# Performance work log

Measured on AMD Instinct MI355X. Metric: run time of the kernel, lower is better.

Reference implementation:

```python
import jax, jax.numpy as jnp
import numpy as np

N_NODES = 50000
N_EDGES = 600000
DIM = 128
NUM_CLASSES = 10
EPS = 1e-15
MAX_NORM = 1.0 - 1e-5  # keep points strictly inside the unit ball for artanh


def _norm(x):
    return jnp.maximum(jnp.linalg.norm(x, axis=-1, keepdims=True), EPS)


def logmap0(x):
    # Poincare ball, c=1: artanh(||x||) * x / ||x||
    n = _norm(x)
    return jnp.arctanh(jnp.minimum(n, MAX_NORM)) * x / n


def expmap0(u):
    # Poincare ball, c=1: tanh(||u||) * u / ||u||
    n = _norm(u)
    return jnp.tanh(n) * u / n


def hyp_conv(x, W, b, src, dst):
    t = logmap0(x)                       # [N, D] manifold -> tangent at origin
    h = t @ W.T + b                      # [N, D] linear in tangent space
    y = expmap0(h)                       # [N, D] back to manifold
    # message passing: gather source features, scatter-add at destinations
    return jax.ops.segment_sum(y[src], dst, num_segments=N_NODES)


def setup_inputs() -> dict:
    key = jax.random.key(0)
    ks = jax.random.split(key, 8)
    edge_index = jax.random.randint(ks[0], (2, N_EDGES), 0, N_NODES, dtype=jnp.int64)
    # entity embeddings: small tangent vectors mapped onto the ball
    x = expmap0(0.01 * jax.random.normal(ks[1], (N_NODES, DIM), dtype=jnp.float32))
    s = 1.0 / np.sqrt(DIM)
    W1 = jax.random.normal(ks[2], (DIM, DIM), dtype=jnp.float32) * s
    b1 = jax.random.normal(ks[3], (DIM,), dtype=jnp.float32) * 0.01
    W2 = jax.random.normal(ks[4], (DIM, DIM), dtype=jnp.float32) * s
    b2 = jax.random.normal(ks[5], (DIM,), dtype=jnp.float32) * 0.01
    Wc = jax.random.normal(ks[6], (NUM_CLASSES, DIM), dtype=jnp.float32) * s
    bc = jax.random.normal(ks[7], (NUM_CLASSES,), dtype=jnp.float32) * 0.01
    return {"edge_index": edge_index, "x": x, "W1": W1, "b1": b1,
            "W2": W2, "b2": b2, "Wc": Wc, "bc": bc}


def reference(edge_index, x, W1, b1, W2, b2, Wc, bc):
    src, dst = edge_index[0], edge_index[1]
    h = hyp_conv(x, W1, b1, src, dst)
    h = jax.nn.relu(h)
    h = hyp_conv(h, W2, b2, src, dst)
    h = jax.nn.relu(h)
    t = logmap0(h)
    return t @ Wc.T + bc  # [N_NODES, NUM_CLASSES]
```

## Files before the change

kernel.cpp:

```cpp
#include <hip/hip_runtime.h>

#define N_NODES 50000
#define N_EDGES 600000
#define DIM 128
#define NCLS 10
#define ELLW 64
#define CURSTRIDE 16
#define EPSF 1e-15f
#define MAXNORM 0.99999f
#define NTILE ((N_NODES + 63) / 64)
#define FILL_BLOCKS 586
#define XFORM_BLOCKS 512

typedef __attribute__((ext_vector_type(8))) short bf16x8;
typedef __attribute__((ext_vector_type(4))) float f32x4;

__device__ inline float waveSum(float v) {
#pragma unroll
  for (int o = 1; o < 64; o <<= 1) v += __shfl_xor(v, o, 64);
  return v;
}

__device__ inline unsigned short f2bf(float f) {
  union { float f; unsigned u; } c; c.f = f;
  return (unsigned short)((c.u + 0x7FFFu + ((c.u >> 16) & 1u)) >> 16);
}
__device__ inline float bf_lo(unsigned u) {
  union { unsigned u; float f; } c; c.u = u << 16; return c.f;
}
__device__ inline float bf_hi(unsigned u) {
  union { unsigned u; float f; } c; c.u = u & 0xFFFF0000u; return c.f;
}

__global__ __launch_bounds__(256) void init_kernel(
    int* __restrict__ cursor, const float* __restrict__ W1, const float* __restrict__ W2,
    unsigned short* __restrict__ W1b, unsigned short* __restrict__ W2b)
{
  int i = blockIdx.x * 256 + threadIdx.x;
  if (i < N_NODES) cursor[i * CURSTRIDE] = 0;
  if (i < DIM * DIM) {
    W1b[i] = f2bf(W1[i]);
    W2b[i] = f2bf(W2[i]);
  }
}

__global__ __launch_bounds__(256, 2) void fill_transform(
    const int* __restrict__ src, const int* __restrict__ dst,
    int* __restrict__ cursor, int* __restrict__ ell,
    const float* __restrict__ x, const unsigned short* __restrict__ Wb,
    const float* __restrict__ b, unsigned short* __restrict__ y)
{
  __shared__ __align__(16) unsigned short At[64 * DIM];

  if (blockIdx.x < FILL_BLOCKS) {
    const int nthr = FILL_BLOCKS * 256;
    const int e = blockIdx.x * 256 + threadIdx.x;
    const int e0 = e, e1 = e + nthr, e2 = e + 2 * nthr, e3 = e + 3 * nthr;
    int d0, d1, d2, d3, s0, s1, s2, s3;
    if (e0 < N_EDGES) { d0 = dst[e0]; s0 = src[e0]; }
    if (e1 < N_EDGES) { d1 = dst[e1]; s1 = src[e1]; }
    if (e2 < N_EDGES) { d2 = dst[e2]; s2 = src[e2]; }
    if (e3 < N_EDGES) { d3 = dst[e3]; s3 = src[e3]; }
    int p0, p1, p2, p3;
    if (e0 < N_EDGES) p0 = atomicAdd(&cursor[d0 * CURSTRIDE], 1);
    if (e1 < N_EDGES) p1 = atomicAdd(&cursor[d1 * CURSTRIDE], 1);
    if (e2 < N_EDGES) p2 = atomicAdd(&cursor[d2 * CURSTRIDE], 1);
    if (e3 < N_EDGES) p3 = atomicAdd(&cursor[d3 * CURSTRIDE], 1);
    if (e0 < N_EDGES) ell[d0 * ELLW + p0] = s0;
    if (e1 < N_EDGES) ell[d1 * ELLW + p1] = s1;
    if (e2 < N_EDGES) ell[d2 * ELLW + p2] = s2;
    if (e3 < N_EDGES) ell[d3 * ELLW + p3] = s3;
    return;
  }

  const int tid = threadIdx.x;
  const int w = tid >> 6;
  const int l = tid & 63;
  const int lr = l & 15;
  const int lg = l >> 4;

  bf16x8 bf[8][4];
#pragma unroll
  for (int n = 0; n < 8; ++n)
#pragma unroll
    for (int kc = 0; kc < 4; ++kc)
      bf[n][kc] = *(const bf16x8*)(Wb + (n * 16 + lr) * DIM + kc * 32 + lg * 8);

  float bias[8];
#pragma unroll
  for (int n = 0; n < 8; ++n) bias[n] = b[n * 16 + lr];

  const int row = w * 16 + lr;

  for (int tile = blockIdx.x - FILL_BLOCKS; tile < NTILE; tile += XFORM_BLOCKS) {
    const int base = tile * 64;
    const int node = base + row;
    __syncthreads();

    float v[32];
    if (node < N_NODES) {
      const float4* xr = (const float4*)(x + (size_t)node * DIM + lg * 32);
#pragma unroll
      for (int q = 0; q < 8; ++q) {
        float4 f = xr[q];
        v[q * 4 + 0] = f.x; v[q * 4 + 1] = f.y; v[q * 4 + 2] = f.z; v[q * 4 + 3] = f.w;
      }
    } else {
#pragma unroll
      for (int q = 0; q < 32; ++q) v[q] = 0.f;
    }
    float sq = 0.f;
#pragma unroll
    for (int q = 0; q < 32; ++q) sq += v[q] * v[q];
    sq += __shfl_xor(sq, 16, 64);
    sq += __shfl_xor(sq, 32, 64);
    float n1 = sqrtf(sq);
    float nc = fmaxf(n1, EPSF);
    float nm = fminf(nc, MAXNORM);
    float scale = 0.5f * logf((1.f + nm) / (1.f - nm)) / nc;
#pragma unroll
    for (int s = 0; s < 4; ++s) {
      unsigned short tmp[8];
#pragma unroll
      for (int e = 0; e < 8; ++e) tmp[e] = f2bf(v[s * 8 + e] * scale);
      int byte = row * 256 + lg * 64 + s * 16;
      byte ^= (row & 7) << 4;
      *(bf16x8*)((char*)At + byte) = *(const bf16x8*)tmp;
    }
    __syncthreads();

    f32x4 acc[8];
#pragma unroll
    for (int n = 0; n < 8; ++n) {
      acc[n][0] = bias[n]; acc[n][1] = bias[n]; acc[n][2] = bias[n]; acc[n][3] = bias[n];
    }
#pragma unroll
    for (int kc = 0; kc < 4; ++kc) {
      int arow = w * 16 + lr;
      int byte = arow * 256 + kc * 64 + lg * 16;
      byte ^= (arow & 7) << 4;
      bf16x8 af = *(const bf16x8*)((const char*)At + byte);
#pragma unroll
      for (int n = 0; n < 8; ++n)
        acc[n] = __builtin_amdgcn_mfma_f32_16x16x32_bf16(af, bf[n][kc], acc[n], 0, 0, 0);
    }

    float rs[4];
#pragma unroll
    for (int j = 0; j < 4; ++j) {
      float s2 = 0.f;
#pragma unroll
      for (int n = 0; n < 8; ++n) s2 += acc[n][j] * acc[n][j];
      s2 += __shfl_xor(s2, 1, 64);
      s2 += __shfl_xor(s2, 2, 64);
      s2 += __shfl_xor(s2, 4, 64);
      s2 += __shfl_xor(s2, 8, 64);
      float n2 = sqrtf(s2);
      float n2c = fmaxf(n2, EPSF);
      rs[j] = tanhf(n2c) / n2c;
    }
#pragma unroll
    for (int j = 0; j < 4; ++j) {
      int nrow = base + w * 16 + lg * 4 + j;
      if (nrow < N_NODES) {
        unsigned short* yr = y + (size_t)nrow * DIM + lr;
#pragma unroll
        for (int n = 0; n < 8; ++n) yr[n * 16] = f2bf(acc[n][j] * rs[j]);
      }
    }
  }
}

__global__ __launch_bounds__(256) void gatherT_kernel(
    const unsigned short* __restrict__ y, const int* __restrict__ cursor,
    const int* __restrict__ ell, unsigned short* __restrict__ tout)
{
  const int node = blockIdx.x * 4 + (threadIdx.x >> 6);
  if (node >= N_NODES) return;
  const int lane = threadIdx.x & 63;
  const int* lst = ell + node * ELLW;
  const int cnt = cursor[node * CURSTRIDE];
  float2 a0 = {0.f, 0.f}, a1 = {0.f, 0.f}, a2 = {0.f, 0.f}, a3 = {0.f, 0.f};
  int j = 0;
  for (; j + 7 < cnt; j += 8) {
    unsigned u0 = ((const unsigned*)(y + (size_t)lst[j    ] * DIM))[lane];
    unsigned u1 = ((const unsigned*)(y + (size_t)lst[j + 1] * DIM))[lane];
    unsigned u2 = ((const unsigned*)(y + (size_t)lst[j + 2] * DIM))[lane];
    unsigned u3 = ((const unsigned*)(y + (size_t)lst[j + 3] * DIM))[lane];
    unsigned u4 = ((const unsigned*)(y + (size_t)lst[j + 4] * DIM))[lane];
    unsigned u5 = ((const unsigned*)(y + (size_t)lst[j + 5] * DIM))[lane];
    unsigned u6 = ((const unsigned*)(y + (size_t)lst[j + 6] * DIM))[lane];
    unsigned u7 = ((const unsigned*)(y + (size_t)lst[j + 7] * DIM))[lane];
    a0.x += bf_lo(u0); a0.y += bf_hi(u0);
    a1.x += bf_lo(u1); a1.y += bf_hi(u1);
    a2.x += bf_lo(u2); a2.y += bf_hi(u2);
    a3.x += bf_lo(u3); a3.y += bf_hi(u3);
    a0.x += bf_lo(u4); a0.y += bf_hi(u4);
    a1.x += bf_lo(u5); a1.y += bf_hi(u5);
    a2.x += bf_lo(u6); a2.y += bf_hi(u6);
    a3.x += bf_lo(u7); a3.y += bf_hi(u7);
  }
  for (; j + 3 < cnt; j += 4) {
    unsigned u0 = ((const unsigned*)(y + (size_t)lst[j    ] * DIM))[lane];
    unsigned u1 = ((const unsigned*)(y + (size_t)lst[j + 1] * DIM))[lane];
    unsigned u2 = ((const unsigned*)(y + (size_t)lst[j + 2] * DIM))[lane];
    unsigned u3 = ((const unsigned*)(y + (size_t)lst[j + 3] * DIM))[lane];
    a0.x += bf_lo(u0); a0.y += bf_hi(u0);
    a1.x += bf_lo(u1); a1.y += bf_hi(u1);
    a2.x += bf_lo(u2); a2.y += bf_hi(u2);
    a3.x += bf_lo(u3); a3.y += bf_hi(u3);
  }
  for (; j < cnt; ++j) {
    unsigned u0 = ((const unsigned*)(y + (size_t)lst[j] * DIM))[lane];
    a0.x += bf_lo(u0); a0.y += bf_hi(u0);
  }
  float2 r;
  r.x = fmaxf((a0.x + a1.x) + (a2.x + a3.x), 0.f);
  r.y = fmaxf((a0.y + a1.y) + (a2.y + a3.y), 0.f);

  float s = waveSum(r.x * r.x + r.y * r.y);
  float n = sqrtf(s);
  float nc = fmaxf(n, EPSF);
  float nm = fminf(nc, MAXNORM);
  float scale = 0.5f * logf((1.0f + nm) / (1.0f - nm)) / nc;
  unsigned u = (unsigned)f2bf(r.x * scale) | ((unsigned)f2bf(r.y * scale) << 16);
  ((unsigned*)(tout + (size_t)node * DIM))[lane] = u;
}

__global__ __launch_bounds__(256, 2) void transform2_mfma(
    const unsigned short* __restrict__ t, const unsigned short* __restrict__ Wb,
    const float* __restrict__ b, unsigned short* __restrict__ y)
{
  const int tid = threadIdx.x;
  const int w = tid >> 6;
  const int l = tid & 63;
  const int lr = l & 15;
  const int lg = l >> 4;

  __shared__ __align__(16) unsigned short At[64 * DIM];

  bf16x8 bf[8][4];
#pragma unroll
  for (int n = 0; n < 8; ++n)
#pragma unroll
    for (int kc = 0; kc < 4; ++kc)
      bf[n][kc] = *(const bf16x8*)(Wb + (n * 16 + lr) * DIM + kc * 32 + lg * 8);

  float bias[8];
#pragma unroll
  for (int n = 0; n < 8; ++n) bias[n] = b[n * 16 + lr];

  const int row = w * 16 + lr;

  for (int tile = blockIdx.x; tile < NTILE; tile += gridDim.x) {
    const int base = tile * 64;
    const int node = base + row;
    __syncthreads();

#pragma unroll
    for (int s = 0; s < 4; ++s) {
      bf16x8 frag;
      if (node < N_NODES)
        frag = *(const bf16x8*)(t + (size_t)node * DIM + lg * 32 + s * 8);
      else
        frag = bf16x8{0, 0, 0, 0, 0, 0, 0, 0};
      int byte = row * 256 + lg * 64 + s * 16;
      byte ^= (row & 7) << 4;
      *(bf16x8*)((char*)At + byte) = frag;
    }
    __syncthreads();

    f32x4 acc[8];
#pragma unroll
    for (int n = 0; n < 8; ++n) {
      acc[n][0] = bias[n]; acc[n][1] = bias[n]; acc[n][2] = bias[n]; acc[n][3] = bias[n];
    }
#pragma unroll
    for (int kc = 0; kc < 4; ++kc) {
      int arow = w * 16 + lr;
      int byte = arow * 256 + kc * 64 + lg * 16;
      byte ^= (arow & 7) << 4;
      bf16x8 af = *(const bf16x8*)((const char*)At + byte);
#pragma unroll
      for (int n = 0; n < 8; ++n)
        acc[n] = __builtin_amdgcn_mfma_f32_16x16x32_bf16(af, bf[n][kc], acc[n], 0, 0, 0);
    }

    float rs[4];
#pragma unroll
    for (int j = 0; j < 4; ++j) {
      float s2 = 0.f;
#pragma unroll
      for (int n = 0; n < 8; ++n) s2 += acc[n][j] * acc[n][j];
      s2 += __shfl_xor(s2, 1, 64);
      s2 += __shfl_xor(s2, 2, 64);
      s2 += __shfl_xor(s2, 4, 64);
      s2 += __shfl_xor(s2, 8, 64);
      float n2 = sqrtf(s2);
      float n2c = fmaxf(n2, EPSF);
      rs[j] = tanhf(n2c) / n2c;
    }
#pragma unroll
    for (int j = 0; j < 4; ++j) {
      int nrow = base + w * 16 + lg * 4 + j;
      if (nrow < N_NODES) {
        unsigned short* yr = y + (size_t)nrow * DIM + lr;
#pragma unroll
        for (int n = 0; n < 8; ++n) yr[n * 16] = f2bf(acc[n][j] * rs[j]);
      }
    }
  }
}

__global__ __launch_bounds__(256) void head_mfma(
    const unsigned short* __restrict__ t2, const float* __restrict__ Wc,
    const float* __restrict__ bc, float* __restrict__ out)
{
  const int base = blockIdx.x * 64;
  const int w = threadIdx.x >> 6;
  const int l = threadIdx.x & 63;
  const int lr = l & 15;
  const int lg = l >> 4;

  bf16x8 bw[4];
#pragma unroll
  for (int kc = 0; kc < 4; ++kc) {
    unsigned short tmp[8];
    if (lr < NCLS) {
      const float* wr = Wc + (size_t)lr * DIM + kc * 32 + lg * 8;
#pragma unroll
      for (int e = 0; e < 8; ++e) tmp[e] = f2bf(wr[e]);
    } else {
#pragma unroll
      for (int e = 0; e < 8; ++e) tmp[e] = 0;
    }
    bw[kc] = *(const bf16x8*)tmp;
  }
  const float bias = (lr < NCLS) ? bc[lr] : 0.f;

  const int arow = base + w * 16 + lr;
  f32x4 acc;
  acc[0] = bias; acc[1] = bias; acc[2] = bias; acc[3] = bias;
#pragma unroll
  for (int kc = 0; kc < 4; ++kc) {
    bf16x8 af;
    if (arow < N_NODES)
      af = *(const bf16x8*)(t2 + (size_t)arow * DIM + kc * 32 + lg * 8);
    else
      af = bf16x8{0, 0, 0, 0, 0, 0, 0, 0};
    acc = __builtin_amdgcn_mfma_f32_16x16x32_bf16(af, bw[kc], acc, 0, 0, 0);
  }

  if (lr < NCLS) {
#pragma unroll
    for (int j = 0; j < 4; ++j) {
      int nrow = base + w * 16 + lg * 4 + j;
      if (nrow < N_NODES) out[(size_t)nrow * NCLS + lr] = acc[j];
    }
  }
}

extern "C" void kernel_launch(void* const* d_in, const int* in_sizes, int n_in,
                              void* d_out, int out_size, void* d_ws, size_t ws_size,
                              hipStream_t stream)
{
  const int* edge = (const int*)d_in[0];
  const int* src = edge;
  const int* dst = edge + N_EDGES;
  const float* x  = (const float*)d_in[1];
  const float* W1 = (const float*)d_in[2];
  const float* b1 = (const float*)d_in[3];
  const float* W2 = (const float*)d_in[4];
  const float* b2 = (const float*)d_in[5];
  const float* Wc = (const float*)d_in[6];
  const float* bc = (const float*)d_in[7];
  float* out = (float*)d_out;

  unsigned short* ybuf = (unsigned short*)d_ws;
  unsigned short* tbuf = ybuf + (size_t)N_NODES * DIM;
  unsigned short* W1b = tbuf + (size_t)N_NODES * DIM;
  unsigned short* W2b = W1b + DIM * DIM;
  int* cursor = (int*)(W2b + DIM * DIM);
  int* ell    = cursor + (size_t)N_NODES * CURSTRIDE;

  init_kernel<<<(N_NODES + 255) / 256, 256, 0, stream>>>(cursor, W1, W2, W1b, W2b);

  fill_transform<<<FILL_BLOCKS + XFORM_BLOCKS, 256, 0, stream>>>(
      src, dst, cursor, ell, x, W1b, b1, ybuf);

  gatherT_kernel<<<(N_NODES + 3) / 4, 256, 0, stream>>>(ybuf, cursor, ell, tbuf);

  transform2_mfma<<<512, 256, 0, stream>>>(tbuf, W2b, b2, ybuf);

  gatherT_kernel<<<(N_NODES + 3) / 4, 256, 0, stream>>>(ybuf, cursor, ell, tbuf);

  head_mfma<<<NTILE, 256, 0, stream>>>(tbuf, Wc, bc, out);
}
```

Before: 135.9 us.

## Fuse neighbor gather with layer-2 transform and classifier head via LDS tiles

Replaces the standalone gather kernels with a device routine that aggregates neighbors for a 64-node tile directly into shared memory. The layer-2 transform and the classifier head now consume that tile, which removes the intermediate tangent buffer round trip and two kernel launches. In exchange, each wave gathers 16 nodes serially with a shallower 4-way unroll, so there is less memory-level parallelism per wave. The new kernels also use only 782 blocks instead of 12500, which may lower gather latency hiding.

```diff
diff --git a/kernel.cpp b/kernel.cpp
--- a/kernel.cpp
+++ b/kernel.cpp
@@ -9,8 +9,8 @@
 #define EPSF 1e-15f
 #define MAXNORM 0.99999f
 #define NTILE ((N_NODES + 63) / 64)
-#define FILL_BLOCKS 586
-#define XFORM_BLOCKS 512
+#define FILLB 586
+#define XFB 512
 
 typedef __attribute__((ext_vector_type(8))) short bf16x8;
 typedef __attribute__((ext_vector_type(4))) float f32x4;
@@ -52,8 +52,8 @@
 {
   __shared__ __align__(16) unsigned short At[64 * DIM];
 
-  if (blockIdx.x < FILL_BLOCKS) {
-    const int nthr = FILL_BLOCKS * 256;
+  if (blockIdx.x < FILLB) {
+    const int nthr = FILLB * 256;
     const int e = blockIdx.x * 256 + threadIdx.x;
     const int e0 = e, e1 = e + nthr, e2 = e + 2 * nthr, e3 = e + 3 * nthr;
     int d0, d1, d2, d3, s0, s1, s2, s3;
@@ -92,7 +92,7 @@
 
   const int row = w * 16 + lr;
 
-  for (int tile = blockIdx.x - FILL_BLOCKS; tile < NTILE; tile += XFORM_BLOCKS) {
+  for (int tile = blockIdx.x - FILLB; tile < NTILE; tile += XFB) {
     const int base = tile * 64;
     const int node = base + row;
     __syncthreads();
@@ -136,9 +136,8 @@
     }
 #pragma unroll
     for (int kc = 0; kc < 4; ++kc) {
-      int arow = w * 16 + lr;
-      int byte = arow * 256 + kc * 64 + lg * 16;
-      byte ^= (arow & 7) << 4;
+      int byte = row * 256 + kc * 64 + lg * 16;
+      byte ^= (row & 7) << 4;
       bf16x8 af = *(const bf16x8*)((const char*)At + byte);
 #pragma unroll
       for (int n = 0; n < 8; ++n)
@@ -171,73 +170,67 @@
   }
 }
 
-__global__ __launch_bounds__(256) void gatherT_kernel(
+__device__ __forceinline__ void gather_tile_to_lds(
     const unsigned short* __restrict__ y, const int* __restrict__ cursor,
-    const int* __restrict__ ell, unsigned short* __restrict__ tout)
-{
-  const int node = blockIdx.x * 4 + (threadIdx.x >> 6);
-  if (node >= N_NODES) return;
-  const int lane = threadIdx.x & 63;
-  const int* lst = ell + node * ELLW;
-  const int cnt = cursor[node * CURSTRIDE];
-  float2 a0 = {0.f, 0.f}, a1 = {0.f, 0.f}, a2 = {0.f, 0.f}, a3 = {0.f, 0.f};
-  int j = 0;
-  for (; j + 7 < cnt; j += 8) {
-    unsigned u0 = ((const unsigned*)(y + (size_t)lst[j    ] * DIM))[lane];
-    unsigned u1 = ((const unsigned*)(y + (size_t)lst[j + 1] * DIM))[lane];
-    unsigned u2 = ((const unsigned*)(y + (size_t)lst[j + 2] * DIM))[lane];
-    unsigned u3 = ((const unsigned*)(y + (size_t)lst[j + 3] * DIM))[lane];
-    unsigned u4 = ((const unsigned*)(y + (size_t)lst[j + 4] * DIM))[lane];
-    unsigned u5 = ((const unsigned*)(y + (size_t)lst[j + 5] * DIM))[lane];
-    unsigned u6 = ((const unsigned*)(y + (size_t)lst[j + 6] * DIM))[lane];
-    unsigned u7 = ((const unsigned*)(y + (size_t)lst[j + 7] * DIM))[lane];
-    a0.x += bf_lo(u0); a0.y += bf_hi(u0);
-    a1.x += bf_lo(u1); a1.y += bf_hi(u1);
-    a2.x += bf_lo(u2); a2.y += bf_hi(u2);
-    a3.x += bf_lo(u3); a3.y += bf_hi(u3);
-    a0.x += bf_lo(u4); a0.y += bf_hi(u4);
-    a1.x += bf_lo(u5); a1.y += bf_hi(u5);
-    a2.x += bf_lo(u6); a2.y += bf_hi(u6);
-    a3.x += bf_lo(u7); a3.y += bf_hi(u7);
-  }
-  for (; j + 3 < cnt; j += 4) {
-    unsigned u0 = ((const unsigned*)(y + (size_t)lst[j    ] * DIM))[lane];
-    unsigned u1 = ((const unsigned*)(y + (size_t)lst[j + 1] * DIM))[lane];
-    unsigned u2 = ((const unsigned*)(y + (size_t)lst[j + 2] * DIM))[lane];
-    unsigned u3 = ((const unsigned*)(y + (size_t)lst[j + 3] * DIM))[lane];
-    a0.x += bf_lo(u0); a0.y += bf_hi(u0);
-    a1.x += bf_lo(u1); a1.y += bf_hi(u1);
-    a2.x += bf_lo(u2); a2.y += bf_hi(u2);
-    a3.x += bf_lo(u3); a3.y += bf_hi(u3);
-  }
-  for (; j < cnt; ++j) {
-    unsigned u0 = ((const unsigned*)(y + (size_t)lst[j] * DIM))[lane];
-    a0.x += bf_lo(u0); a0.y += bf_hi(u0);
-  }
-  float2 r;
-  r.x = fmaxf((a0.x + a1.x) + (a2.x + a3.x), 0.f);
-  r.y = fmaxf((a0.y + a1.y) + (a2.y + a3.y), 0.f);
-
-  float s = waveSum(r.x * r.x + r.y * r.y);
-  float n = sqrtf(s);
-  float nc = fmaxf(n, EPSF);
-  float nm = fminf(nc, MAXNORM);
-  float scale = 0.5f * logf((1.0f + nm) / (1.0f - nm)) / nc;
-  unsigned u = (unsigned)f2bf(r.x * scale) | ((unsigned)f2bf(r.y * scale) << 16);
-  ((unsigned*)(tout + (size_t)node * DIM))[lane] = u;
-}
-
-__global__ __launch_bounds__(256, 2) void transform2_mfma(
-    const unsigned short* __restrict__ t, const unsigned short* __restrict__ Wb,
-    const float* __restrict__ b, unsigned short* __restrict__ y)
-{
+    const int* __restrict__ ell, unsigned short* At, int base, int w, int l)
+{
+  const int wrow = w * 16;
+#pragma unroll 1
+  for (int k = 0; k < 16; ++k) {
+    const int node = base + wrow + k;
+    float ax = 0.f, ay = 0.f, bx = 0.f, by = 0.f;
+    float cx = 0.f, cy = 0.f, dx = 0.f, dy = 0.f;
+    if (node < N_NODES) {
+      const int cnt = cursor[node * CURSTRIDE];
+      const int* lst = ell + (size_t)node * ELLW;
+      int j = 0;
+      for (; j + 3 < cnt; j += 4) {
+        unsigned u0 = ((const unsigned*)(y + (size_t)lst[j    ] * DIM))[l];
+        unsigned u1 = ((const unsigned*)(y + (size_t)lst[j + 1] * DIM))[l];
+        unsigned u2 = ((const unsigned*)(y + (size_t)lst[j + 2] * DIM))[l];
+        unsigned u3 = ((const unsigned*)(y + (size_t)lst[j + 3] * DIM))[l];
+        ax += bf_lo(u0); ay += bf_hi(u0);
+        bx += bf_lo(u1); by += bf_hi(u1);
+        cx += bf_lo(u2); cy += bf_hi(u2);
+        dx += bf_lo(u3); dy += bf_hi(u3);
+      }
+      for (; j < cnt; ++j) {
+        unsigned u0 = ((const unsigned*)(y + (size_t)lst[j] * DIM))[l];
+        ax += bf_lo(u0); ay += bf_hi(u0);
+      }
+    }
+    float rx = fmaxf((ax + bx) + (cx + dx), 0.f);
+    float ry = fmaxf((ay + by) + (cy + dy), 0.f);
+
+    float s = waveSum(rx * rx + ry * ry);
+    float n = sqrtf(s);
+    float ncl = fmaxf(n, EPSF);
+    float nm = fminf(ncl, MAXNORM);
+    float scale = 0.5f * logf((1.f + nm) / (1.f - nm)) / ncl;
+
+    const int row = wrow + k;
+    int byte = row * 256 + l * 4;
+    byte ^= (row & 7) << 4;
+    unsigned u = (unsigned)f2bf(rx * scale) | ((unsigned)f2bf(ry * scale) << 16);
+    *(unsigned*)((char*)At + byte) = u;
+  }
+}
+
+__global__ __launch_bounds__(256, 2) void gather_t2(
+    const unsigned short* __restrict__ y, const int* __restrict__ cursor,
+    const int* __restrict__ ell, const unsigned short* __restrict__ Wb,
+    const float* __restrict__ b, unsigned short* __restrict__ y2)
+{
+  __shared__ __align__(16) unsigned short At[64 * DIM];
   const int tid = threadIdx.x;
   const int w = tid >> 6;
   const int l = tid & 63;
   const int lr = l & 15;
   const int lg = l >> 4;
-
-  __shared__ __align__(16) unsigned short At[64 * DIM];
+  const int base = blockIdx.x * 64;
+
+  gather_tile_to_lds(y, cursor, ell, At, base, w, l);
+  __syncthreads();
 
   bf16x8 bf[8][4];
 #pragma unroll
@@ -251,76 +244,61 @@
   for (int n = 0; n < 8; ++n) bias[n] = b[n * 16 + lr];
 
   const int row = w * 16 + lr;
-
-  for (int tile = blockIdx.x; tile < NTILE; tile += gridDim.x) {
-    const int base = tile * 64;
-    const int node = base + row;
-    __syncthreads();
-
-#pragma unroll
-    for (int s = 0; s < 4; ++s) {
-      bf16x8 frag;
-      if (node < N_NODES)
-        frag = *(const bf16x8*)(t + (size_t)node * DIM + lg * 32 + s * 8);
-      else
-        frag = bf16x8{0, 0, 0, 0, 0, 0, 0, 0};
-      int byte = row * 256 + lg * 64 + s * 16;
-      byte ^= (row & 7) << 4;
-      *(bf16x8*)((char*)At + byte) = frag;
-    }
-    __syncthreads();
-
-    f32x4 acc[8];
-#pragma unroll
-    for (int n = 0; n < 8; ++n) {
-      acc[n][0] = bias[n]; acc[n][1] = bias[n]; acc[n][2] = bias[n]; acc[n][3] = bias[n];
-    }
-#pragma unroll
-    for (int kc = 0; kc < 4; ++kc) {
-      int arow = w * 16 + lr;
-      int byte = arow * 256 + kc * 64 + lg * 16;
-      byte ^= (arow & 7) << 4;
-      bf16x8 af = *(const bf16x8*)((const char*)At + byte);
-#pragma unroll
-      for (int n = 0; n < 8; ++n)
-        acc[n] = __builtin_amdgcn_mfma_f32_16x16x32_bf16(af, bf[n][kc], acc[n], 0, 0, 0);
-    }
-
-    float rs[4];
-#pragma unroll
-    for (int j = 0; j < 4; ++j) {
-      float s2 = 0.f;
-#pragma unroll
-      for (int n = 0; n < 8; ++n) s2 += acc[n][j] * acc[n][j];
-      s2 += __shfl_xor(s2, 1, 64);
-      s2 += __shfl_xor(s2, 2, 64);
-      s2 += __shfl_xor(s2, 4, 64);
-      s2 += __shfl_xor(s2, 8, 64);
-      float n2 = sqrtf(s2);
-      float n2c = fmaxf(n2, EPSF);
-      rs[j] = tanhf(n2c) / n2c;
-    }
-#pragma unroll
-    for (int j = 0; j < 4; ++j) {
-      int nrow = base + w * 16 + lg * 4 + j;
-      if (nrow < N_NODES) {
-        unsigned short* yr = y + (size_t)nrow * DIM + lr;
-#pragma unroll
-        for (int n = 0; n < 8; ++n) yr[n * 16] = f2bf(acc[n][j] * rs[j]);
-      }
-    }
-  }
-}
-
-__global__ __launch_bounds__(256) void head_mfma(
-    const unsigned short* __restrict__ t2, const float* __restrict__ Wc,
+  f32x4 acc[8];
+#pragma unroll
+  for (int n = 0; n < 8; ++n) {
+    acc[n][0] = bias[n]; acc[n][1] = bias[n]; acc[n][2] = bias[n]; acc[n][3] = bias[n];
+  }
+#pragma unroll
+  for (int kc = 0; kc < 4; ++kc) {
+    int byte = row * 256 + kc * 64 + lg * 16;
+    byte ^= (row & 7) << 4;
+    bf16x8 af = *(const bf16x8*)((const char*)At + byte);
+#pragma unroll
+    for (int n = 0; n < 8; ++n)
+      acc[n] = __builtin_amdgcn_mfma_f32_16x16x32_bf16(af, bf[n][kc], acc[n], 0, 0, 0);
+  }
+
+  float rs[4];
+#pragma unroll
+  for (int j = 0; j < 4; ++j) {
+    float s2 = 0.f;
+#pragma unroll
+    for (int n = 0; n < 8; ++n) s2 += acc[n][j] * acc[n][j];
+    s2 += __shfl_xor(s2, 1, 64);
+    s2 += __shfl_xor(s2, 2, 64);
+    s2 += __shfl_xor(s2, 4, 64);
+    s2 += __shfl_xor(s2, 8, 64);
+    float n2 = sqrtf(s2);
+    float n2c = fmaxf(n2, EPSF);
+    rs[j] = tanhf(n2c) / n2c;
+  }
+#pragma unroll
+  for (int j = 0; j < 4; ++j) {
+    int nrow = base + w * 16 + lg * 4 + j;
+    if (nrow < N_NODES) {
+      unsigned short* yr = y2 + (size_t)nrow * DIM + lr;
+#pragma unroll
+      for (int n = 0; n < 8; ++n) yr[n * 16] = f2bf(acc[n][j] * rs[j]);
+    }
+  }
+}
+
+__global__ __launch_bounds__(256, 2) void gather_head(
+    const unsigned short* __restrict__ y2, const int* __restrict__ cursor,
+    const int* __restrict__ ell, const float* __restrict__ Wc,
     const float* __restrict__ bc, float* __restrict__ out)
 {
-  const int base = blockIdx.x * 64;
-  const int w = threadIdx.x >> 6;
-  const int l = threadIdx.x & 63;
+  __shared__ __align__(16) unsigned short At[64 * DIM];
+  const int tid = threadIdx.x;
+  const int w = tid >> 6;
+  const int l = tid & 63;
   const int lr = l & 15;
   const int lg = l >> 4;
+  const int base = blockIdx.x * 64;
+
+  gather_tile_to_lds(y2, cursor, ell, At, base, w, l);
+  __syncthreads();
 
   bf16x8 bw[4];
 #pragma unroll
@@ -338,16 +316,14 @@
   }
   const float bias = (lr < NCLS) ? bc[lr] : 0.f;
 
-  const int arow = base + w * 16 + lr;
+  const int row = w * 16 + lr;
   f32x4 acc;
   acc[0] = bias; acc[1] = bias; acc[2] = bias; acc[3] = bias;
 #pragma unroll
   for (int kc = 0; kc < 4; ++kc) {
-    bf16x8 af;
-    if (arow < N_NODES)
-      af = *(const bf16x8*)(t2 + (size_t)arow * DIM + kc * 32 + lg * 8);
-    else
-      af = bf16x8{0, 0, 0, 0, 0, 0, 0, 0};
+    int byte = row * 256 + kc * 64 + lg * 16;
+    byte ^= (row & 7) << 4;
+    bf16x8 af = *(const bf16x8*)((const char*)At + byte);
     acc = __builtin_amdgcn_mfma_f32_16x16x32_bf16(af, bw[kc], acc, 0, 0, 0);
   }
 
@@ -376,23 +352,18 @@
   const float* bc = (const float*)d_in[7];
   float* out = (float*)d_out;
 
-  unsigned short* ybuf = (unsigned short*)d_ws;
-  unsigned short* tbuf = ybuf + (size_t)N_NODES * DIM;
-  unsigned short* W1b = tbuf + (size_t)N_NODES * DIM;
+  unsigned short* ybuf  = (unsigned short*)d_ws;
+  unsigned short* y2buf = ybuf + (size_t)N_NODES * DIM;
+  unsigned short* W1b = y2buf + (size_t)N_NODES * DIM;
   unsigned short* W2b = W1b + DIM * DIM;
   int* cursor = (int*)(W2b + DIM * DIM);
-  int* ell    = cursor + (size_t)N_NODES * CURSTRIDE;
+  int* ell = cursor + (size_t)N_NODES * CURSTRIDE;
 
   init_kernel<<<(N_NODES + 255) / 256, 256, 0, stream>>>(cursor, W1, W2, W1b, W2b);
 
-  fill_transform<<<FILL_BLOCKS + XFORM_BLOCKS, 256, 0, stream>>>(
-      src, dst, cursor, ell, x, W1b, b1, ybuf);
-
-  gatherT_kernel<<<(N_NODES + 3) / 4, 256, 0, stream>>>(ybuf, cursor, ell, tbuf);
-
-  transform2_mfma<<<512, 256, 0, stream>>>(tbuf, W2b, b2, ybuf);
-
-  gatherT_kernel<<<(N_NODES + 3) / 4, 256, 0, stream>>>(ybuf, cursor, ell, tbuf);
-
-  head_mfma<<<NTILE, 256, 0, stream>>>(tbuf, Wc, bc, out);
-}
+  fill_transform<<<FILLB + XFB, 256, 0, stream>>>(src, dst, cursor, ell, x, W1b, b1, ybuf);
+
+  gather_t2<<<NTILE, 256, 0, stream>>>(ybuf, cursor, ell, W2b, b2, y2buf);
+
+  gather_head<<<NTILE, 256, 0, stream>>>(y2buf, cursor, ell, Wc, bc, out);
+}
```

After: 183.7 us. +35.2%, slower.
